# Kernel optimization log

Hardware: AMD Instinct MI355X
Metric: run time of the kernel (lower is better)

The kernel has to match this reference:

```python
import jax, jax.numpy as jnp
import numpy as np

B, S, D, H = 8, 2048, 512, 2
DK = D  # per-head dim (d_k=d_v=in_dim in source)
OUT = 512
EPS = 1e-5


def setup_inputs() -> dict:
    key = jax.random.key(0)
    ks = jax.random.split(key, 20)
    sc = lambda fan_in: 1.0 / np.sqrt(fan_in)
    inp = {
        "x": jax.random.normal(ks[0], (B, S, D), jnp.float32),
        "skip": jax.random.normal(ks[1], (B, S, D), jnp.float32),
        # attention projections: d_model -> h*d_k
        "Wq": jax.random.normal(ks[2], (H * DK, D), jnp.float32) * sc(D),
        "bq": jnp.zeros((H * DK,), jnp.float32),
        "Wk": jax.random.normal(ks[3], (H * DK, D), jnp.float32) * sc(D),
        "bk": jnp.zeros((H * DK,), jnp.float32),
        "Wv": jax.random.normal(ks[4], (H * DK, D), jnp.float32) * sc(D),
        "bv": jnp.zeros((H * DK,), jnp.float32),
        "Wo": jax.random.normal(ks[5], (D, H * DK), jnp.float32) * sc(H * DK),
        "bo": jnp.zeros((D,), jnp.float32),
        # post linear in_dim -> out_dim
        "Wl": jax.random.normal(ks[6], (OUT, D), jnp.float32) * sc(D),
        "bl": jnp.zeros((OUT,), jnp.float32),
        # LayerNorm params
        "gamma": jnp.ones((OUT,), jnp.float32),
        "beta": jnp.zeros((OUT,), jnp.float32),
        # proj(skip): Linear(512 -> out_dim)
        "Wp": jax.random.normal(ks[7], (OUT, D), jnp.float32) * sc(D),
        "bp": jnp.zeros((OUT,), jnp.float32),
    }
    return inp


def _upblock(x, skip, Wq, bq, Wk, bk, Wv, bv, Wo, bo, Wl, bl, gamma, beta, Wp, bp):
    # multi-head scaled dot-product self-attention (hand-rolled, as in source)
    q = (x @ Wq.T + bq).reshape(B, S, H, DK)  # bshd
    k = (x @ Wk.T + bk).reshape(B, S, H, DK)
    v = (x @ Wv.T + bv).reshape(B, S, H, DK)
    scores = jnp.einsum("bqhd,bkhd->bhqk", q, k) / jnp.sqrt(jnp.float32(DK))
    att = jax.nn.softmax(scores, axis=-1)
    o = jnp.einsum("bhqk,bkhd->bqhd", att, v).reshape(B, S, H * DK)
    o = o @ Wo.T + bo  # [B,S,D]
    # SiLU -> Linear -> LayerNorm
    h = jax.nn.silu(o) @ Wl.T + bl  # [B,S,OUT]
    mu = jnp.mean(h, axis=-1, keepdims=True)
    var = jnp.mean(jnp.square(h - mu), axis=-1, keepdims=True)
    h = (h - mu) * jax.lax.rsqrt(var + EPS) * gamma + beta
    # residual with projected skip
    return h + (skip @ Wp.T + bp)


def reference(x, skip, Wq, bq, Wk, bk, Wv, bv, Wo, bo, Wl, bl, gamma, beta, Wp, bp):
    return _upblock(x, skip, Wq, bq, Wk, bk, Wv, bv, Wo, bo, Wl, bl, gamma, beta, Wp, bp)
```

## Files before the change

### kernel.cpp

```cpp
#include <hip/hip_runtime.h>
#include <math.h>

typedef unsigned short u16;
typedef u16 u16x8 __attribute__((ext_vector_type(8)));
typedef __bf16 bf16x8 __attribute__((ext_vector_type(8)));
typedef float f32x4 __attribute__((ext_vector_type(4)));

#define MBL (1LL << 20)

__device__ __forceinline__ u16 f2bf(float x) {
    unsigned u = __float_as_uint(x);
    return (u16)((u + 0x7fffu + ((u >> 16) & 1u)) >> 16);
}
__device__ __forceinline__ float bf2f(u16 h) { return __uint_as_float(((unsigned)h) << 16); }
__device__ __forceinline__ float silu_f(float x) { return x / (1.f + __expf(-x)); }

template<int EPI>
__global__ __launch_bounds__(256)
void gemm_sp(const float* __restrict__ Af, const float* __restrict__ Bf,
             float* __restrict__ Cf,
             long lda, long ldb, long ldc, int K, float alpha,
             const float* __restrict__ bias,
             const float* __restrict__ addp, long ldadd,
             int zbase,
             long sAb, long sAh2, long sAz,
             long sBb, long sBh2, long sBz,
             long sCb, long sCh2, long sCz)
{
    const int z = blockIdx.z, bh = zbase + z, zb = bh >> 1, zh = bh & 1;
    Af += (long)zb * sAb + (long)zh * sAh2 + (long)z * sAz;
    Bf += (long)zb * sBb + (long)zh * sBh2 + (long)z * sBz;
    Cf += (long)zb * sCb + (long)zh * sCh2 + (long)z * sCz;

    __shared__ u16 As[2][128 * 32];
    __shared__ u16 Bs[2][128 * 32];

    const int tid = threadIdx.x;
    const int wave = tid >> 6, lane = tid & 63;
    const long m0 = (long)blockIdx.y * 128;
    const long n0 = (long)blockIdx.x * 128;

    const int srow = tid >> 1;
    const int sh   = (tid & 1) << 4;
    const float* gA = Af + (m0 + srow) * lda + sh;
    const float* gB = Bf + (n0 + srow) * ldb + sh;
    const int sBase = srow * 32 + sh;

    const int wr = (wave >> 1) << 6;
    const int wc = (wave & 1) << 6;
    const int fr = lane & 15;
    const int fk = (lane >> 4) << 3;

    f32x4 acc[4][4];
#pragma unroll
    for (int i = 0; i < 4; ++i)
#pragma unroll
        for (int j = 0; j < 4; ++j) acc[i][j] = (f32x4)0.f;

    for (int kb = 0; kb < K; kb += 32) {
        float a[16], b[16];
        *(float4*)&a[0]  = *(const float4*)(gA + kb);
        *(float4*)&a[4]  = *(const float4*)(gA + kb + 4);
        *(float4*)&a[8]  = *(const float4*)(gA + kb + 8);
        *(float4*)&a[12] = *(const float4*)(gA + kb + 12);
        *(float4*)&b[0]  = *(const float4*)(gB + kb);
        *(float4*)&b[4]  = *(const float4*)(gB + kb + 4);
        *(float4*)&b[8]  = *(const float4*)(gB + kb + 8);
        *(float4*)&b[12] = *(const float4*)(gB + kb + 12);
        u16 ahv[16], alv[16], bhv[16], blv[16];
#pragma unroll
        for (int u = 0; u < 16; ++u) {
            u16 h = f2bf(a[u]); ahv[u] = h; alv[u] = f2bf(a[u] - bf2f(h));
            u16 g = f2bf(b[u]); bhv[u] = g; blv[u] = f2bf(b[u] - bf2f(g));
        }
        __syncthreads();
        *(u16x8*)&As[0][sBase]     = *(u16x8*)&ahv[0];
        *(u16x8*)&As[0][sBase + 8] = *(u16x8*)&ahv[8];
        *(u16x8*)&As[1][sBase]     = *(u16x8*)&alv[0];
        *(u16x8*)&As[1][sBase + 8] = *(u16x8*)&alv[8];
        *(u16x8*)&Bs[0][sBase]     = *(u16x8*)&bhv[0];
        *(u16x8*)&Bs[0][sBase + 8] = *(u16x8*)&bhv[8];
        *(u16x8*)&Bs[1][sBase]     = *(u16x8*)&blv[0];
        *(u16x8*)&Bs[1][sBase + 8] = *(u16x8*)&blv[8];
        __syncthreads();

        bf16x8 ah[4], al[4], bh8[4], bl8[4];
#pragma unroll
        for (int i = 0; i < 4; ++i) {
            const int r = (wr + (i << 4) + fr) * 32 + fk;
            ah[i] = *(const bf16x8*)&As[0][r];
            al[i] = *(const bf16x8*)&As[1][r];
        }
#pragma unroll
        for (int j = 0; j < 4; ++j) {
            const int r = (wc + (j << 4) + fr) * 32 + fk;
            bh8[j] = *(const bf16x8*)&Bs[0][r];
            bl8[j] = *(const bf16x8*)&Bs[1][r];
        }
#pragma unroll
        for (int i = 0; i < 4; ++i)
#pragma unroll
            for (int j = 0; j < 4; ++j) {
                acc[i][j] = __builtin_amdgcn_mfma_f32_16x16x32_bf16(ah[i], bh8[j], acc[i][j], 0, 0, 0);
                acc[i][j] = __builtin_amdgcn_mfma_f32_16x16x32_bf16(ah[i], bl8[j], acc[i][j], 0, 0, 0);
                acc[i][j] = __builtin_amdgcn_mfma_f32_16x16x32_bf16(al[i], bh8[j], acc[i][j], 0, 0, 0);
            }
    }

    const int rl = (lane >> 4) << 2;
#pragma unroll
    for (int j = 0; j < 4; ++j) {
        const long col = n0 + wc + (j << 4) + fr;
        const float bb = bias ? bias[col] : 0.f;
#pragma unroll
        for (int i = 0; i < 4; ++i) {
#pragma unroll
            for (int r2 = 0; r2 < 4; ++r2) {
                const long row = m0 + wr + (i << 4) + rl + r2;
                float c = acc[i][j][r2] * alpha + bb;
                if (EPI == 1) c = silu_f(c);
                if (EPI == 2) c += addp[row * ldadd + col];
                Cf[row * ldc + col] = c;
            }
        }
    }
}

__global__ __launch_bounds__(256)
void transpose_vf(const float* __restrict__ v, float* __restrict__ vt)
{
    const int z = blockIdx.z;
    const int ib = z >> 1, h = z & 1;
    const float* src = v + (long)ib * 2097152 + (long)h * 512;
    float* dst = vt + (long)z * 1048576;
    __shared__ float T[64][68];
    const int t = threadIdx.x;
    const int r = t >> 2, c0 = (t & 3) << 4;
    const long sBase = (long)blockIdx.x * 64;
    const long dBase = (long)blockIdx.y * 64;
    const float* sp = src + (sBase + r) * 1024 + dBase + c0;
#pragma unroll
    for (int q = 0; q < 4; ++q)
        *(float4*)&T[r][c0 + 4 * q] = *(const float4*)(sp + 4 * q);
    __syncthreads();
    float* dp = dst + (dBase + r) * 2048 + sBase + c0;
#pragma unroll
    for (int q = 0; q < 4; ++q) {
        float4 o;
        o.x = T[c0 + 4 * q + 0][r]; o.y = T[c0 + 4 * q + 1][r];
        o.z = T[c0 + 4 * q + 2][r]; o.w = T[c0 + 4 * q + 3][r];
        *(float4*)(dp + 4 * q) = o;
    }
}

__global__ __launch_bounds__(256)
void softmax_rows(float* __restrict__ P)
{
    const int lane = threadIdx.x & 63;
    const long row = ((long)blockIdx.x << 2) + (threadIdx.x >> 6);
    float* pr = P + row * 2048;
    float4 xv[8];
#pragma unroll
    for (int i = 0; i < 8; ++i) xv[i] = *(const float4*)(pr + (lane << 2) + (i << 8));
    float m = -3.4e38f;
#pragma unroll
    for (int i = 0; i < 8; ++i)
        m = fmaxf(m, fmaxf(fmaxf(xv[i].x, xv[i].y), fmaxf(xv[i].z, xv[i].w)));
#pragma unroll
    for (int off = 32; off >= 1; off >>= 1) m = fmaxf(m, __shfl_xor(m, off));
    float s = 0.f;
#pragma unroll
    for (int i = 0; i < 8; ++i) {
        xv[i].x = __expf(xv[i].x - m); xv[i].y = __expf(xv[i].y - m);
        xv[i].z = __expf(xv[i].z - m); xv[i].w = __expf(xv[i].w - m);
        s += xv[i].x + xv[i].y + xv[i].z + xv[i].w;
    }
#pragma unroll
    for (int off = 32; off >= 1; off >>= 1) s += __shfl_xor(s, off);
    const float r = 1.f / s;
#pragma unroll
    for (int i = 0; i < 8; ++i) {
        xv[i].x *= r; xv[i].y *= r; xv[i].z *= r; xv[i].w *= r;
        *(float4*)(pr + (lane << 2) + (i << 8)) = xv[i];
    }
}

__global__ __launch_bounds__(256)
void layernorm_rows(const float* __restrict__ h,
                    const float* __restrict__ gamma,
                    const float* __restrict__ beta,
                    float* __restrict__ o)
{
    const int lane = threadIdx.x & 63;
    const long row = ((long)blockIdx.x << 2) + (threadIdx.x >> 6);
    const float* hr = h + row * 512;
    float v[8];
    *(float4*)&v[0] = *(const float4*)(hr + (lane << 3));
    *(float4*)&v[4] = *(const float4*)(hr + (lane << 3) + 4);
    float s = 0.f;
#pragma unroll
    for (int i = 0; i < 8; ++i) s += v[i];
#pragma unroll
    for (int off = 32; off >= 1; off >>= 1) s += __shfl_xor(s, off);
    const float mu = s * (1.f / 512.f);
    float sq = 0.f;
#pragma unroll
    for (int i = 0; i < 8; ++i) { v[i] -= mu; sq = fmaf(v[i], v[i], sq); }
#pragma unroll
    for (int off = 32; off >= 1; off >>= 1) sq += __shfl_xor(sq, off);
    const float rs = rsqrtf(sq * (1.f / 512.f) + 1e-5f);
    float g[8], b[8];
    *(float4*)&g[0] = *(const float4*)(gamma + (lane << 3));
    *(float4*)&g[4] = *(const float4*)(gamma + (lane << 3) + 4);
    *(float4*)&b[0] = *(const float4*)(beta + (lane << 3));
    *(float4*)&b[4] = *(const float4*)(beta + (lane << 3) + 4);
    float ov[8];
#pragma unroll
    for (int i = 0; i < 8; ++i) ov[i] = fmaf(v[i] * rs, g[i], b[i]);
    float* orow = o + row * 512;
    *(float4*)(orow + (lane << 3))     = *(float4*)&ov[0];
    *(float4*)(orow + (lane << 3) + 4) = *(float4*)&ov[4];
}

extern "C" void kernel_launch(void* const* d_in, const int* in_sizes, int n_in,
                              void* d_out, int out_size, void* d_ws, size_t ws_size,
                              hipStream_t stream)
{
    const float* x    = (const float*)d_in[0];
    const float* skip = (const float*)d_in[1];
    const float* Wq   = (const float*)d_in[2];
    const float* bq   = (const float*)d_in[3];
    const float* Wk   = (const float*)d_in[4];
    const float* bk   = (const float*)d_in[5];
    const float* Wv   = (const float*)d_in[6];
    const float* bv   = (const float*)d_in[7];
    const float* Wo   = (const float*)d_in[8];
    const float* bo   = (const float*)d_in[9];
    const float* Wl   = (const float*)d_in[10];
    const float* bl   = (const float*)d_in[11];
    const float* gm   = (const float*)d_in[12];
    const float* bt   = (const float*)d_in[13];
    const float* Wp   = (const float*)d_in[14];
    const float* bp   = (const float*)d_in[15];
    float* out = (float*)d_out;

    long gbl = (long)(ws_size / (64 * MBL));
    int gb = gbl < 1 ? 1 : (gbl > 8 ? 8 : (int)gbl);

    float* ws  = (float*)d_ws;
    const long G = gb;
    float* qb  = ws;
    float* kb_ = ws + G * 2097152;
    float* vb  = ws + 2 * G * 2097152;
    float* vtb = ws + 3 * G * 2097152;
    float* scb = ws + 4 * G * 2097152;
    float* oproj = qb;
    float* hb    = kb_;
    float* lnh   = vtb;

    const float sscale = 0.044194173824159216f;
    const long Z = 0;

    for (int b0 = 0; b0 < 8; b0 += gb) {
        const int gc = (8 - b0) < gb ? (8 - b0) : gb;
        gemm_sp<0><<<dim3(8, gc * 16, 1), 256, 0, stream>>>(
            x + (long)b0 * 1048576, Wq, qb, 512, 512, 1024, 512, 1.f, bq,
            nullptr, 0, 0, Z,Z,Z, Z,Z,Z, Z,Z,Z);
        gemm_sp<0><<<dim3(8, gc * 16, 1), 256, 0, stream>>>(
            x + (long)b0 * 1048576, Wk, kb_, 512, 512, 1024, 512, 1.f, bk,
            nullptr, 0, 0, Z,Z,Z, Z,Z,Z, Z,Z,Z);
        gemm_sp<0><<<dim3(8, gc * 16, 1), 256, 0, stream>>>(
            x + (long)b0 * 1048576, Wv, vb, 512, 512, 1024, 512, 1.f, bv,
            nullptr, 0, 0, Z,Z,Z, Z,Z,Z, Z,Z,Z);
        transpose_vf<<<dim3(32, 8, 2 * gc), 256, 0, stream>>>(vb, vtb);
        gemm_sp<0><<<dim3(16, 16, 2 * gc), 256, 0, stream>>>(
            qb - (long)b0 * 2097152, kb_ - (long)b0 * 2097152, scb,
            1024, 1024, 2048, 512, sscale, nullptr, nullptr, 0, 2 * b0,
            2097152L, 512, Z, 2097152L, 512, Z, Z, Z, 4194304L);
        softmax_rows<<<dim3(gc * 1024), 256, 0, stream>>>(scb);
        gemm_sp<0><<<dim3(4, 16, 2 * gc), 256, 0, stream>>>(
            scb, vtb, vb - (long)b0 * 2097152,
            2048, 2048, 1024, 2048, 1.f, nullptr, nullptr, 0, 2 * b0,
            Z, Z, 4194304L, Z, Z, 1048576L, 2097152L, 512, Z);
        gemm_sp<1><<<dim3(4, gc * 16, 1), 256, 0, stream>>>(
            vb, Wo, oproj, 1024, 1024, 512, 1024, 1.f, bo,
            nullptr, 0, 0, Z,Z,Z, Z,Z,Z, Z,Z,Z);
        gemm_sp<0><<<dim3(4, gc * 16, 1), 256, 0, stream>>>(
            oproj, Wl, hb, 512, 512, 512, 512, 1.f, bl,
            nullptr, 0, 0, Z,Z,Z, Z,Z,Z, Z,Z,Z);
        layernorm_rows<<<dim3(gc * 512), 256, 0, stream>>>(hb, gm, bt, lnh);
        gemm_sp<2><<<dim3(4, gc * 16, 1), 256, 0, stream>>>(
            skip + (long)b0 * 1048576, Wp, out + (long)b0 * 1048576,
            512, 512, 512, 512, 1.f, bp, lnh, 512, 0, Z,Z,Z, Z,Z,Z, Z,Z,Z);
    }
}
```

Before: 1.375 ms.

## Pre-split operands to bf16 hi/lo, fuse softmax into GEMM epilogues, use global_load_lds

Weights and intermediate activations are now stored pre-split into bf16 hi/lo pairs. GEMMs load these directly into LDS via global_load_lds instead of converting fp32 inside every tile iteration. Softmax is folded into the QK^T epilogue (exp with atomic row sums) and the PV epilogue (divide by the row sum). The later projection GEMMs run once over the whole batch instead of per group. The softmax drops the max subtraction, so it relies on scores being small enough not to overflow exp, and the atomics add nondeterminism.

```diff
diff --git a/kernel.cpp b/kernel.cpp
--- a/kernel.cpp
+++ b/kernel.cpp
@@ -15,36 +15,47 @@
 __device__ __forceinline__ float bf2f(u16 h) { return __uint_as_float(((unsigned)h) << 16); }
 __device__ __forceinline__ float silu_f(float x) { return x / (1.f + __expf(-x)); }
 
-template<int EPI>
+#define GLDS(gp, off) __builtin_amdgcn_global_load_lds( \
+    (const __attribute__((address_space(1))) void*)(gp), \
+    (__attribute__((address_space(3))) void*)(&SL[off]), 16, 0, 0)
+
+template<int SPLITA, int EPI>
 __global__ __launch_bounds__(256)
-void gemm_sp(const float* __restrict__ Af, const float* __restrict__ Bf,
-             float* __restrict__ Cf,
+void gemm_ss(const float* __restrict__ Af,
+             const u16* __restrict__ Ah, const u16* __restrict__ Al,
+             const u16* __restrict__ Bh, const u16* __restrict__ Bl,
+             float* __restrict__ Cf, u16* __restrict__ Ch, u16* __restrict__ Cl,
+             float* __restrict__ rsum,
              long lda, long ldb, long ldc, int K, float alpha,
              const float* __restrict__ bias,
              const float* __restrict__ addp, long ldadd,
-             int zbase,
-             long sAb, long sAh2, long sAz,
-             long sBb, long sBh2, long sBz,
-             long sCb, long sCh2, long sCz)
-{
-    const int z = blockIdx.z, bh = zbase + z, zb = bh >> 1, zh = bh & 1;
-    Af += (long)zb * sAb + (long)zh * sAh2 + (long)z * sAz;
-    Bf += (long)zb * sBb + (long)zh * sBh2 + (long)z * sBz;
-    Cf += (long)zb * sCb + (long)zh * sCh2 + (long)z * sCz;
-
-    __shared__ u16 As[2][128 * 32];
-    __shared__ u16 Bs[2][128 * 32];
+             long sAb, long sAh2, long sBb, long sBh2, long sCb, long sCh2)
+{
+    const int z = blockIdx.z, zb = z >> 1, zh = z & 1;
+    const long offA = (long)zb * sAb + (long)zh * sAh2;
+    const long offB = (long)zb * sBb + (long)zh * sBh2;
+    const long offC = (long)zb * sCb + (long)zh * sCh2;
+    if (SPLITA) { Ah += offA; Al += offA; } else { Af += offA; }
+    Bh += offB; Bl += offB;
+    if (EPI == 0) Cf += offC; else { Ch += offC; Cl += offC; }
+    if (EPI >= 3) rsum += (long)z * 2048;
+
+    __shared__ u16 SL[16384];
+    const int AH = 0, AL = 4096, BH = 8192, BL = 12288;
 
     const int tid = threadIdx.x;
     const int wave = tid >> 6, lane = tid & 63;
     const long m0 = (long)blockIdx.y * 128;
     const long n0 = (long)blockIdx.x * 128;
 
+    const int lrow = lane >> 2;
+    const int kcol = (lane & 3) << 3;
+    const int ldsW = wave * 512;
+
     const int srow = tid >> 1;
     const int sh   = (tid & 1) << 4;
-    const float* gA = Af + (m0 + srow) * lda + sh;
-    const float* gB = Bf + (n0 + srow) * ldb + sh;
-    const int sBase = srow * 32 + sh;
+    const float* gA = SPLITA ? nullptr : (Af + (m0 + srow) * lda + sh);
+    const int sB = srow * 32 + sh;
 
     const int wr = (wave >> 1) << 6;
     const int wc = (wave & 1) << 6;
@@ -58,81 +69,129 @@
         for (int j = 0; j < 4; ++j) acc[i][j] = (f32x4)0.f;
 
     for (int kb = 0; kb < K; kb += 32) {
-        float a[16], b[16];
-        *(float4*)&a[0]  = *(const float4*)(gA + kb);
-        *(float4*)&a[4]  = *(const float4*)(gA + kb + 4);
-        *(float4*)&a[8]  = *(const float4*)(gA + kb + 8);
-        *(float4*)&a[12] = *(const float4*)(gA + kb + 12);
-        *(float4*)&b[0]  = *(const float4*)(gB + kb);
-        *(float4*)&b[4]  = *(const float4*)(gB + kb + 4);
-        *(float4*)&b[8]  = *(const float4*)(gB + kb + 8);
-        *(float4*)&b[12] = *(const float4*)(gB + kb + 12);
-        u16 ahv[16], alv[16], bhv[16], blv[16];
-#pragma unroll
-        for (int u = 0; u < 16; ++u) {
-            u16 h = f2bf(a[u]); ahv[u] = h; alv[u] = f2bf(a[u] - bf2f(h));
-            u16 g = f2bf(b[u]); bhv[u] = g; blv[u] = f2bf(b[u] - bf2f(g));
+        float a[16];
+        if (!SPLITA) {
+            *(float4*)&a[0]  = *(const float4*)(gA + kb);
+            *(float4*)&a[4]  = *(const float4*)(gA + kb + 4);
+            *(float4*)&a[8]  = *(const float4*)(gA + kb + 8);
+            *(float4*)&a[12] = *(const float4*)(gA + kb + 12);
         }
         __syncthreads();
-        *(u16x8*)&As[0][sBase]     = *(u16x8*)&ahv[0];
-        *(u16x8*)&As[0][sBase + 8] = *(u16x8*)&ahv[8];
-        *(u16x8*)&As[1][sBase]     = *(u16x8*)&alv[0];
-        *(u16x8*)&As[1][sBase + 8] = *(u16x8*)&alv[8];
-        *(u16x8*)&Bs[0][sBase]     = *(u16x8*)&bhv[0];
-        *(u16x8*)&Bs[0][sBase + 8] = *(u16x8*)&bhv[8];
-        *(u16x8*)&Bs[1][sBase]     = *(u16x8*)&blv[0];
-        *(u16x8*)&Bs[1][sBase + 8] = *(u16x8*)&blv[8];
+#pragma unroll
+        for (int t = 0; t < 2; ++t) {
+            const long row = wave * 16 + lrow + t * 64;
+            GLDS(Bh + (n0 + row) * ldb + kb + kcol, BH + ldsW + t * 2048);
+            GLDS(Bl + (n0 + row) * ldb + kb + kcol, BL + ldsW + t * 2048);
+            if (SPLITA) {
+                GLDS(Ah + (m0 + row) * lda + kb + kcol, AH + ldsW + t * 2048);
+                GLDS(Al + (m0 + row) * lda + kb + kcol, AL + ldsW + t * 2048);
+            }
+        }
+        if (!SPLITA) {
+            u16 hv[16], lv[16];
+#pragma unroll
+            for (int u = 0; u < 16; ++u) {
+                u16 h = f2bf(a[u]); hv[u] = h; lv[u] = f2bf(a[u] - bf2f(h));
+            }
+            *(u16x8*)&SL[AH + sB]     = *(u16x8*)&hv[0];
+            *(u16x8*)&SL[AH + sB + 8] = *(u16x8*)&hv[8];
+            *(u16x8*)&SL[AL + sB]     = *(u16x8*)&lv[0];
+            *(u16x8*)&SL[AL + sB + 8] = *(u16x8*)&lv[8];
+        }
         __syncthreads();
 
-        bf16x8 ah[4], al[4], bh8[4], bl8[4];
+        bf16x8 fah[4], fal[4], fbh[4], fbl[4];
 #pragma unroll
         for (int i = 0; i < 4; ++i) {
             const int r = (wr + (i << 4) + fr) * 32 + fk;
-            ah[i] = *(const bf16x8*)&As[0][r];
-            al[i] = *(const bf16x8*)&As[1][r];
+            fah[i] = *(const bf16x8*)&SL[AH + r];
+            fal[i] = *(const bf16x8*)&SL[AL + r];
         }
 #pragma unroll
         for (int j = 0; j < 4; ++j) {
             const int r = (wc + (j << 4) + fr) * 32 + fk;
-            bh8[j] = *(const bf16x8*)&Bs[0][r];
-            bl8[j] = *(const bf16x8*)&Bs[1][r];
+            fbh[j] = *(const bf16x8*)&SL[BH + r];
+            fbl[j] = *(const bf16x8*)&SL[BL + r];
         }
 #pragma unroll
         for (int i = 0; i < 4; ++i)
 #pragma unroll
             for (int j = 0; j < 4; ++j) {
-                acc[i][j] = __builtin_amdgcn_mfma_f32_16x16x32_bf16(ah[i], bh8[j], acc[i][j], 0, 0, 0);
-                acc[i][j] = __builtin_amdgcn_mfma_f32_16x16x32_bf16(ah[i], bl8[j], acc[i][j], 0, 0, 0);
-                acc[i][j] = __builtin_amdgcn_mfma_f32_16x16x32_bf16(al[i], bh8[j], acc[i][j], 0, 0, 0);
+                acc[i][j] = __builtin_amdgcn_mfma_f32_16x16x32_bf16(fah[i], fbh[j], acc[i][j], 0, 0, 0);
+                acc[i][j] = __builtin_amdgcn_mfma_f32_16x16x32_bf16(fah[i], fbl[j], acc[i][j], 0, 0, 0);
+                acc[i][j] = __builtin_amdgcn_mfma_f32_16x16x32_bf16(fal[i], fbh[j], acc[i][j], 0, 0, 0);
             }
     }
 
     const int rl = (lane >> 4) << 2;
 #pragma unroll
-    for (int j = 0; j < 4; ++j) {
-        const long col = n0 + wc + (j << 4) + fr;
-        const float bb = bias ? bias[col] : 0.f;
-#pragma unroll
-        for (int i = 0; i < 4; ++i) {
-#pragma unroll
-            for (int r2 = 0; r2 < 4; ++r2) {
-                const long row = m0 + wr + (i << 4) + rl + r2;
-                float c = acc[i][j][r2] * alpha + bb;
-                if (EPI == 1) c = silu_f(c);
-                if (EPI == 2) c += addp[row * ldadd + col];
-                Cf[row * ldc + col] = c;
+    for (int i = 0; i < 4; ++i) {
+#pragma unroll
+        for (int r2 = 0; r2 < 4; ++r2) {
+            const long row = m0 + wr + (i << 4) + rl + r2;
+            float psum = 0.f;
+            float rinv = 0.f;
+            if (EPI == 4) rinv = 1.f / rsum[row];
+#pragma unroll
+            for (int j = 0; j < 4; ++j) {
+                const long col = n0 + wc + (j << 4) + fr;
+                float c = acc[i][j][r2];
+                if (EPI == 0 || EPI == 1 || EPI == 2) {
+                    c = c * alpha + (bias ? bias[col] : 0.f);
+                }
+                if (EPI == 0) {
+                    if (addp) c += addp[row * ldadd + col];
+                    Cf[row * ldc + col] = c;
+                } else if (EPI == 1 || EPI == 2) {
+                    if (EPI == 2) c = silu_f(c);
+                    u16 h = f2bf(c);
+                    Ch[row * ldc + col] = h;
+                    Cl[row * ldc + col] = f2bf(c - bf2f(h));
+                } else if (EPI == 3) {
+                    float p = __expf(c * alpha);
+                    psum += p;
+                    u16 h = f2bf(p);
+                    Ch[row * ldc + col] = h;
+                    Cl[row * ldc + col] = f2bf(p - bf2f(h));
+                } else {
+                    c *= rinv;
+                    u16 h = f2bf(c);
+                    Ch[row * ldc + col] = h;
+                    Cl[row * ldc + col] = f2bf(c - bf2f(h));
+                }
+            }
+            if (EPI == 3) {
+                psum += __shfl_xor(psum, 1);
+                psum += __shfl_xor(psum, 2);
+                psum += __shfl_xor(psum, 4);
+                psum += __shfl_xor(psum, 8);
+                if ((lane & 15) == 0) atomicAdd(&rsum[row], psum);
             }
         }
     }
 }
 
 __global__ __launch_bounds__(256)
-void transpose_vf(const float* __restrict__ v, float* __restrict__ vt)
-{
-    const int z = blockIdx.z;
-    const int ib = z >> 1, h = z & 1;
-    const float* src = v + (long)ib * 2097152 + (long)h * 512;
-    float* dst = vt + (long)z * 1048576;
+void split_f32(const float* __restrict__ in, u16* __restrict__ hi, u16* __restrict__ lo)
+{
+    const long i = (((long)blockIdx.x << 8) + threadIdx.x) << 3;
+    float4 v0 = *(const float4*)(in + i), v1 = *(const float4*)(in + i + 4);
+    float f[8] = {v0.x, v0.y, v0.z, v0.w, v1.x, v1.y, v1.z, v1.w};
+    u16x8 h8, l8;
+#pragma unroll
+    for (int u = 0; u < 8; ++u) { u16 h = f2bf(f[u]); h8[u] = h; l8[u] = f2bf(f[u] - bf2f(h)); }
+    *(u16x8*)(hi + i) = h8;
+    *(u16x8*)(lo + i) = l8;
+}
+
+__global__ __launch_bounds__(256)
+void transpose_vs(const float* __restrict__ v, u16* __restrict__ vth, u16* __restrict__ vtl,
+                  long sVb, long sVh, long sTb, long sTh)
+{
+    const int z = blockIdx.z, s = z >> 1, h = z & 1;
+    const float* src = v + (long)s * sVb + (long)h * sVh;
+    u16* dh = vth + (long)s * sTb + (long)h * sTh;
+    u16* dl = vtl + (long)s * sTb + (long)h * sTh;
     __shared__ float T[64][68];
     const int t = threadIdx.x;
     const int r = t >> 2, c0 = (t & 3) << 4;
@@ -143,46 +202,18 @@
     for (int q = 0; q < 4; ++q)
         *(float4*)&T[r][c0 + 4 * q] = *(const float4*)(sp + 4 * q);
     __syncthreads();
-    float* dp = dst + (dBase + r) * 2048 + sBase + c0;
-#pragma unroll
-    for (int q = 0; q < 4; ++q) {
-        float4 o;
-        o.x = T[c0 + 4 * q + 0][r]; o.y = T[c0 + 4 * q + 1][r];
-        o.z = T[c0 + 4 * q + 2][r]; o.w = T[c0 + 4 * q + 3][r];
-        *(float4*)(dp + 4 * q) = o;
-    }
-}
-
-__global__ __launch_bounds__(256)
-void softmax_rows(float* __restrict__ P)
-{
-    const int lane = threadIdx.x & 63;
-    const long row = ((long)blockIdx.x << 2) + (threadIdx.x >> 6);
-    float* pr = P + row * 2048;
-    float4 xv[8];
-#pragma unroll
-    for (int i = 0; i < 8; ++i) xv[i] = *(const float4*)(pr + (lane << 2) + (i << 8));
-    float m = -3.4e38f;
-#pragma unroll
-    for (int i = 0; i < 8; ++i)
-        m = fmaxf(m, fmaxf(fmaxf(xv[i].x, xv[i].y), fmaxf(xv[i].z, xv[i].w)));
-#pragma unroll
-    for (int off = 32; off >= 1; off >>= 1) m = fmaxf(m, __shfl_xor(m, off));
-    float s = 0.f;
-#pragma unroll
-    for (int i = 0; i < 8; ++i) {
-        xv[i].x = __expf(xv[i].x - m); xv[i].y = __expf(xv[i].y - m);
-        xv[i].z = __expf(xv[i].z - m); xv[i].w = __expf(xv[i].w - m);
-        s += xv[i].x + xv[i].y + xv[i].z + xv[i].w;
-    }
-#pragma unroll
-    for (int off = 32; off >= 1; off >>= 1) s += __shfl_xor(s, off);
-    const float r = 1.f / s;
-#pragma unroll
-    for (int i = 0; i < 8; ++i) {
-        xv[i].x *= r; xv[i].y *= r; xv[i].z *= r; xv[i].w *= r;
-        *(float4*)(pr + (lane << 2) + (i << 8)) = xv[i];
-    }
+    u16x8 h8[2], l8[2];
+#pragma unroll
+    for (int g = 0; g < 2; ++g)
+#pragma unroll
+        for (int u = 0; u < 8; ++u) {
+            float f = T[c0 + g * 8 + u][r];
+            u16 h = f2bf(f);
+            h8[g][u] = h; l8[g][u] = f2bf(f - bf2f(h));
+        }
+    const long o = (dBase + r) * 2048 + sBase + c0;
+    *(u16x8*)&dh[o] = h8[0]; *(u16x8*)&dh[o + 8] = h8[1];
+    *(u16x8*)&dl[o] = l8[0]; *(u16x8*)&dl[o + 8] = l8[1];
 }
 
 __global__ __launch_bounds__(256)
@@ -244,53 +275,86 @@
     const float* bp   = (const float*)d_in[15];
     float* out = (float*)d_out;
 
-    long gbl = (long)(ws_size / (64 * MBL));
+    char* W = (char*)d_ws;
+    u16* wqh = (u16*)(W);
+    u16* wql = wqh + 524288;
+    u16* wkh = wql + 524288;  u16* wkl = wkh + 524288;
+    u16* wvh = wkl + 524288;  u16* wvl = wvh + 524288;
+    u16* woh = wvl + 524288;  u16* wol = woh + 524288;
+    u16* wlh = wol + 524288;  u16* wll = wlh + 262144;
+    u16* wph = wll + 262144;  u16* wpl = wph + 262144;
+    float* rsum = (float*)(W + 10 * MBL);
+    u16* ahi  = (u16*)(W + 16 * MBL);
+    u16* alo  = (u16*)(W + 48 * MBL);
+    u16* ophi = (u16*)(W + 80 * MBL);
+    u16* oplo = (u16*)(W + 96 * MBL);
+    float* hb  = (float*)(W + 16 * MBL);
+    float* lnh = (float*)(W + 48 * MBL);
+    char* PB = W + 112 * MBL;
+
+    long avail = (long)ws_size - 112 * MBL;
+    long gbl = avail / (56 * MBL);
     int gb = gbl < 1 ? 1 : (gbl > 8 ? 8 : (int)gbl);
 
-    float* ws  = (float*)d_ws;
-    const long G = gb;
-    float* qb  = ws;
-    float* kb_ = ws + G * 2097152;
-    float* vb  = ws + 2 * G * 2097152;
-    float* vtb = ws + 3 * G * 2097152;
-    float* scb = ws + 4 * G * 2097152;
-    float* oproj = qb;
-    float* hb    = kb_;
-    float* lnh   = vtb;
+    const long SLOT_U = 29360128;
+    const long SLOT_F = 14680064;
+    u16*   qh0 = (u16*)(PB);
+    u16*   kh0 = (u16*)(PB + 8 * MBL);
+    u16*   vth0 = (u16*)(PB + 16 * MBL);
+    u16*   ph0 = (u16*)(PB + 24 * MBL);
+    float* vtm0 = (float*)(PB + 24 * MBL);
 
     const float sscale = 0.044194173824159216f;
     const long Z = 0;
 
+    hipMemsetAsync(rsum, 0, 16 * 2048 * 4, stream);
+
+    split_f32<<<256, 256, 0, stream>>>(Wq, wqh, wql);
+    split_f32<<<256, 256, 0, stream>>>(Wk, wkh, wkl);
+    split_f32<<<256, 256, 0, stream>>>(Wv, wvh, wvl);
+    split_f32<<<256, 256, 0, stream>>>(Wo, woh, wol);
+    split_f32<<<128, 256, 0, stream>>>(Wl, wlh, wll);
+    split_f32<<<128, 256, 0, stream>>>(Wp, wph, wpl);
+
     for (int b0 = 0; b0 < 8; b0 += gb) {
         const int gc = (8 - b0) < gb ? (8 - b0) : gb;
-        gemm_sp<0><<<dim3(8, gc * 16, 1), 256, 0, stream>>>(
-            x + (long)b0 * 1048576, Wq, qb, 512, 512, 1024, 512, 1.f, bq,
-            nullptr, 0, 0, Z,Z,Z, Z,Z,Z, Z,Z,Z);
-        gemm_sp<0><<<dim3(8, gc * 16, 1), 256, 0, stream>>>(
-            x + (long)b0 * 1048576, Wk, kb_, 512, 512, 1024, 512, 1.f, bk,
-            nullptr, 0, 0, Z,Z,Z, Z,Z,Z, Z,Z,Z);
-        gemm_sp<0><<<dim3(8, gc * 16, 1), 256, 0, stream>>>(
-            x + (long)b0 * 1048576, Wv, vb, 512, 512, 1024, 512, 1.f, bv,
-            nullptr, 0, 0, Z,Z,Z, Z,Z,Z, Z,Z,Z);
-        transpose_vf<<<dim3(32, 8, 2 * gc), 256, 0, stream>>>(vb, vtb);
-        gemm_sp<0><<<dim3(16, 16, 2 * gc), 256, 0, stream>>>(
-            qb - (long)b0 * 2097152, kb_ - (long)b0 * 2097152, scb,
-            1024, 1024, 2048, 512, sscale, nullptr, nullptr, 0, 2 * b0,
-            2097152L, 512, Z, 2097152L, 512, Z, Z, Z, 4194304L);
-        softmax_rows<<<dim3(gc * 1024), 256, 0, stream>>>(scb);
-        gemm_sp<0><<<dim3(4, 16, 2 * gc), 256, 0, stream>>>(
-            scb, vtb, vb - (long)b0 * 2097152,
-            2048, 2048, 1024, 2048, 1.f, nullptr, nullptr, 0, 2 * b0,
-            Z, Z, 4194304L, Z, Z, 1048576L, 2097152L, 512, Z);
-        gemm_sp<1><<<dim3(4, gc * 16, 1), 256, 0, stream>>>(
-            vb, Wo, oproj, 1024, 1024, 512, 1024, 1.f, bo,
-            nullptr, 0, 0, Z,Z,Z, Z,Z,Z, Z,Z,Z);
-        gemm_sp<0><<<dim3(4, gc * 16, 1), 256, 0, stream>>>(
-            oproj, Wl, hb, 512, 512, 512, 512, 1.f, bl,
-            nullptr, 0, 0, Z,Z,Z, Z,Z,Z, Z,Z,Z);
-        layernorm_rows<<<dim3(gc * 512), 256, 0, stream>>>(hb, gm, bt, lnh);
-        gemm_sp<2><<<dim3(4, gc * 16, 1), 256, 0, stream>>>(
-            skip + (long)b0 * 1048576, Wp, out + (long)b0 * 1048576,
-            512, 512, 512, 512, 1.f, bp, lnh, 512, 0, Z,Z,Z, Z,Z,Z, Z,Z,Z);
+        const float* xg = x + (long)b0 * 1048576;
+        gemm_ss<0, 1><<<dim3(8, 16, gc), 256, 0, stream>>>(
+            xg, nullptr, nullptr, wqh, wql, nullptr, qh0, qh0 + 2097152, nullptr,
+            512, 512, 1024, 512, 1.f, bq, nullptr, 0,
+            2097152L, 1048576L, Z, Z, 2 * SLOT_U, SLOT_U);
+        gemm_ss<0, 1><<<dim3(8, 16, gc), 256, 0, stream>>>(
+            xg, nullptr, nullptr, wkh, wkl, nullptr, kh0, kh0 + 2097152, nullptr,
+            512, 512, 1024, 512, 1.f, bk, nullptr, 0,
+            2097152L, 1048576L, Z, Z, 2 * SLOT_U, SLOT_U);
+        gemm_ss<0, 0><<<dim3(8, 16, gc), 256, 0, stream>>>(
+            xg, nullptr, nullptr, wvh, wvl, vtm0, nullptr, nullptr, nullptr,
+            512, 512, 1024, 512, 1.f, bv, nullptr, 0,
+            2097152L, 1048576L, Z, Z, 2 * SLOT_F, SLOT_F);
+        transpose_vs<<<dim3(32, 8, 2 * gc), 256, 0, stream>>>(
+            vtm0, vth0, vth0 + 1048576,
+            SLOT_F, 512, SLOT_U, 2097152L);
+        gemm_ss<1, 3><<<dim3(16, 16, 2 * gc), 256, 0, stream>>>(
+            nullptr, qh0, qh0 + 2097152, kh0, kh0 + 2097152,
+            nullptr, ph0, ph0 + 2048, rsum + (long)b0 * 4096,
+            1024, 1024, 4096, 512, sscale, nullptr, nullptr, 0,
+            SLOT_U, 512, SLOT_U, 512, SLOT_U, 8388608L);
+        gemm_ss<1, 4><<<dim3(4, 16, 2 * gc), 256, 0, stream>>>(
+            nullptr, ph0, ph0 + 2048, vth0, vth0 + 1048576,
+            nullptr, ahi + (long)b0 * 2097152, alo + (long)b0 * 2097152,
+            rsum + (long)b0 * 4096,
+            4096, 2048, 1024, 2048, 1.f, nullptr, nullptr, 0,
+            SLOT_U, 8388608L, SLOT_U, 2097152L, 2097152L, 512);
     }
-}
+
+    gemm_ss<1, 2><<<dim3(4, 128, 1), 256, 0, stream>>>(
+        nullptr, ahi, alo, woh, wol, nullptr, ophi, oplo, nullptr,
+        1024, 1024, 512, 1024, 1.f, bo, nullptr, 0, Z, Z, Z, Z, Z, Z);
+    gemm_ss<1, 0><<<dim3(4, 128, 1), 256, 0, stream>>>(
+        nullptr, ophi, oplo, wlh, wll, hb, nullptr, nullptr, nullptr,
+        512, 512, 512, 512, 1.f, bl, nullptr, 0, Z, Z, Z, Z, Z, Z);
+    layernorm_rows<<<4096, 256, 0, stream>>>(hb, gm, bt, lnh);
+    gemm_ss<0, 0><<<dim3(4, 128, 1), 256, 0, stream>>>(
+        skip, nullptr, nullptr, wph, wpl, out, nullptr, nullptr, nullptr,
+        512, 512, 512, 512, 1.f, bp, lnh, 512, Z, Z, Z, Z, Z, Z);
+}
```

Result: slower. 1.450 ms (+5.5%).
